# Kernel tuning notes

Measured on AMD Instinct MI355X. Metric: run time of the kernel, lower is better.

## Reference

```python
import jax, jax.numpy as jnp
import numpy as np

SEQ_LEN = 2048
DIM = 1024
HEADS = 16
DIM_HEAD = 64
INNER = HEADS * DIM_HEAD
BASE = 10000.0


def rope_tables(seq_len, head_dim):
    inv_freq = 1.0 / (BASE ** (jnp.arange(0, head_dim, 2, dtype=jnp.float32) / head_dim))
    t = jnp.arange(seq_len, dtype=jnp.float32)
    freqs = jnp.einsum('i,j->ij', t, inv_freq)          # [n, d/2]
    emb = jnp.concatenate([freqs, freqs], axis=-1)       # [n, d]
    return jnp.cos(emb), jnp.sin(emb)                    # each [n, d]


def rotate_half(x):
    d = x.shape[-1] // 2
    return jnp.concatenate([-x[..., d:], x[..., :d]], axis=-1)


def setup_inputs() -> dict:
    key = jax.random.key(0)
    ks = jax.random.split(key, 5)
    x = jax.random.normal(ks[0], (2, SEQ_LEN, DIM), dtype=jnp.float32)
    W_qkv = jax.random.normal(ks[1], (DIM, 3 * INNER), dtype=jnp.float32) * (DIM ** -0.5)
    W_out = jax.random.normal(ks[2], (INNER, DIM), dtype=jnp.float32) * (INNER ** -0.5)
    b_out = jnp.zeros((DIM,), dtype=jnp.float32)
    ln_g = jnp.ones((DIM,), dtype=jnp.float32)
    ln_b = jnp.zeros((DIM,), dtype=jnp.float32)
    return {"x": x, "W_qkv": W_qkv, "W_out": W_out, "b_out": b_out, "ln_g": ln_g, "ln_b": ln_b}


def reference(x, W_qkv, W_out, b_out, ln_g, ln_b):
    b, n, _ = x.shape
    # LayerNorm
    mu = jnp.mean(x, axis=-1, keepdims=True)
    var = jnp.mean(jnp.square(x - mu), axis=-1, keepdims=True)
    xn = (x - mu) * jax.lax.rsqrt(var + 1e-5) * ln_g + ln_b
    # QKV projection -> [b, h, n, d]
    qkv = xn @ W_qkv                                   # [b, n, 3*inner]
    q, k, v = jnp.split(qkv, 3, axis=-1)
    def to_heads(t):
        return t.reshape(b, n, HEADS, DIM_HEAD).transpose(0, 2, 1, 3)
    q, k, v = to_heads(q), to_heads(k), to_heads(v)
    # RoPE
    cos, sin = rope_tables(n, DIM_HEAD)                # [n, d]
    cos = cos[None, None]                              # [1,1,n,d]
    sin = sin[None, None]
    q = q * cos + rotate_half(q) * sin
    k = k * cos + rotate_half(k) * sin
    # Attention
    scale = DIM_HEAD ** -0.5
    dots = jnp.einsum('bhid,bhjd->bhij', q, k) * scale  # [b,h,n,n]
    causal = jnp.tril(jnp.ones((n, n), dtype=bool))
    dots = jnp.where(causal[None, None], dots, jnp.float32(-jnp.inf))
    attn = jax.nn.softmax(dots, axis=-1)
    out = jnp.einsum('bhij,bhjd->bhid', attn, v)       # [b,h,n,d]
    out = out.transpose(0, 2, 1, 3).reshape(b, n, INNER)
    return out @ W_out + b_out
```

## Files before the change

### kernel.cpp

```cpp
#include <hip/hip_runtime.h>
#include <hip/hip_bf16.h>

#define SEQ    2048
#define DMODEL 1024
#define HEADS  16
#define DHEAD  64
#define BATCH  2
#define TOK    (BATCH * SEQ)
#define NQKV   (3 * DMODEL)
#define QK_SCALE (0.125f * 1.4426950408889634f)

typedef __attribute__((ext_vector_type(8))) short bf16x8;
typedef __attribute__((ext_vector_type(4))) float f32x4;

__device__ __forceinline__ float bf2f(ushort u) {
  union { unsigned int i; float f; } v; v.i = ((unsigned int)u) << 16; return v.f;
}
__device__ __forceinline__ ushort f2bf(float f) {
  union { float f; unsigned int i; } v; v.f = f;
  unsigned int r = (v.i + 0x7fffu + ((v.i >> 16) & 1u)) >> 16;
  return (ushort)r;
}

__device__ __forceinline__ int swz(int row, int byteoff) {
  return row * 128 + (byteoff ^ ((row & 7) << 4));
}
__device__ __forceinline__ int kperm(int s) {
  return (s & 0x20) | ((s & 0x0C) << 1) | ((s & 0x10) >> 2) | (s & 3);
}

#define GLL16(g, l)                                                                     \
  __builtin_amdgcn_global_load_lds((const __attribute__((address_space(1))) void*)(g),  \
                                   (__attribute__((address_space(3))) void*)(l), 16, 0, 0)

__global__ __launch_bounds__(256) void ln_kernel(const float* __restrict__ x,
                                                 const float* __restrict__ g,
                                                 const float* __restrict__ b,
                                                 ushort* __restrict__ xn) {
  int t = blockIdx.x;
  int tid = threadIdx.x;
  const float* row = x + (size_t)t * DMODEL;
  float4 v = *(const float4*)(row + tid * 4);
  float s  = v.x + v.y + v.z + v.w;
  float s2 = v.x * v.x + v.y * v.y + v.z * v.z + v.w * v.w;
#pragma unroll
  for (int m = 32; m >= 1; m >>= 1) {
    s  += __shfl_down(s, m);
    s2 += __shfl_down(s2, m);
  }
  __shared__ float ws[4], ws2[4];
  if ((tid & 63) == 0) { ws[tid >> 6] = s; ws2[tid >> 6] = s2; }
  __syncthreads();
  s  = ws[0] + ws[1] + ws[2] + ws[3];
  s2 = ws2[0] + ws2[1] + ws2[2] + ws2[3];
  float mu  = s * (1.f / DMODEL);
  float var = s2 * (1.f / DMODEL) - mu * mu;
  float rs  = rsqrtf(var + 1e-5f);
  float4 gv = *(const float4*)(g + tid * 4);
  float4 bv = *(const float4*)(b + tid * 4);
  ushort4 o;
  o.x = f2bf((v.x - mu) * rs * gv.x + bv.x);
  o.y = f2bf((v.y - mu) * rs * gv.y + bv.y);
  o.z = f2bf((v.z - mu) * rs * gv.z + bv.z);
  o.w = f2bf((v.w - mu) * rs * gv.w + bv.w);
  *(ushort4*)(xn + (size_t)t * DMODEL + tid * 4) = o;
}

__global__ void transpose_f2b(const float* __restrict__ in, ushort* __restrict__ out,
                              int R, int C) {
  __shared__ float tile[32][33];
  int c0 = blockIdx.x * 32, r0 = blockIdx.y * 32;
  int x = threadIdx.x, y = threadIdx.y;
#pragma unroll
  for (int i = 0; i < 32; i += 8) tile[y + i][x] = in[(size_t)(r0 + y + i) * C + c0 + x];
  __syncthreads();
#pragma unroll
  for (int i = 0; i < 32; i += 8) out[(size_t)(c0 + y + i) * R + r0 + x] = f2bf(tile[x][y + i]);
}

__global__ void rope_tab_kernel(float* __restrict__ ct, float* __restrict__ st) {
  int n = blockIdx.x, d = threadIdx.x;
  float invf = expf(-logf(10000.f) * (float)(d & 31) * (1.f / 32.f));
  float a = (float)n * invf;
  ct[n * DHEAD + d] = cosf(a);
  st[n * DHEAD + d] = sinf(a);
}

template<int EPI>
__global__ __launch_bounds__(256) void gemm_bt(const ushort* __restrict__ A,
                                               const ushort* __restrict__ BT,
                                               float* __restrict__ Cf,
                                               const float* __restrict__ bias,
                                               ushort* __restrict__ qh,
                                               ushort* __restrict__ kh,
                                               ushort* __restrict__ vh,
                                               const float* __restrict__ ct,
                                               const float* __restrict__ st,
                                               int M, int N, int K) {
  __shared__ __align__(16) ushort As[128 * 64];
  __shared__ __align__(16) ushort Bs[128 * 64];
  int tid = threadIdx.x;
  int w = tid >> 6, lane = tid & 63;
  int lrow = lane & 15, g = lane >> 4;
  int gx = gridDim.x;
  int wg = blockIdx.x + gx * blockIdx.y;
  int nwg = gx * gridDim.y;
  int cpx = nwg >> 3;
  int swg = (wg & 7) * cpx + (wg >> 3);
  int m0 = (swg / gx) * 128, n0 = (swg % gx) * 128;
  int wr = (w >> 1) * 64, wc = (w & 1) * 64;
  int r8 = lane >> 3, s8 = lane & 7;
  int scol = (s8 ^ r8) * 8;
  f32x4 acc[4][4] = {};
  for (int k0 = 0; k0 < K; k0 += 64) {
    __syncthreads();
#pragma unroll
    for (int c = 0; c < 4; c++) {
      int row = w * 32 + c * 8;
      GLL16(A  + (size_t)(m0 + row + r8) * K + k0 + scol, As + row * 64);
      GLL16(BT + (size_t)(n0 + row + r8) * K + k0 + scol, Bs + row * 64);
    }
    __syncthreads();
#pragma unroll
    for (int ks = 0; ks < 2; ks++) {
      bf16x8 af[4], bf[4];
#pragma unroll
      for (int i = 0; i < 4; i++) {
        int ra = wr + i * 16 + lrow;
        af[i] = *(const bf16x8*)((const char*)As + swz(ra, g * 16 + ks * 64));
        int rb = wc + i * 16 + lrow;
        bf[i] = *(const bf16x8*)((const char*)Bs + swz(rb, g * 16 + ks * 64));
      }
      __builtin_amdgcn_s_setprio(1);
#pragma unroll
      for (int mf = 0; mf < 4; mf++)
#pragma unroll
        for (int nf = 0; nf < 4; nf++)
          acc[mf][nf] = __builtin_amdgcn_mfma_f32_16x16x32_bf16(af[mf], bf[nf], acc[mf][nf], 0, 0, 0);
      __builtin_amdgcn_s_setprio(0);
    }
  }
#pragma unroll
  for (int mf = 0; mf < 4; mf++)
#pragma unroll
    for (int nf = 0; nf < 4; nf++) {
      int col = n0 + wc + nf * 16 + lrow;
#pragma unroll
      for (int r = 0; r < 4; r++) {
        int rowi = m0 + wr + mf * 16 + g * 4 + r;
        float val = acc[mf][nf][r];
        if (EPI == 2) {
          Cf[(size_t)rowi * N + col] = val + bias[col];
        } else {
          int mat = col >> 10, c1 = col & 1023;
          int h = c1 >> 6, d = c1 & 63;
          int bb = rowi >> 11, n = rowi & (SEQ - 1);
          if (mat < 2) {
            float partner = acc[mf][nf ^ 2][r];
            float cs = ct[n * DHEAD + d], sn = st[n * DHEAD + d];
            float sgn = (d & 32) ? 1.f : -1.f;
            val = val * cs + sgn * partner * sn;
            if (mat == 0) val *= QK_SCALE;
          }
          ushort* dst = (mat == 0) ? qh : (mat == 1) ? kh : vh;
          dst[((size_t)(bb * HEADS + h) * SEQ + n) * DHEAD + d] = f2bf(val);
        }
      }
    }
}

__global__ __launch_bounds__(256) void attn_kernel(const ushort* __restrict__ q,
                                                   const ushort* __restrict__ k,
                                                   const ushort* __restrict__ v,
                                                   ushort* __restrict__ ao) {
  int wgid = blockIdx.x + gridDim.x * blockIdx.y;
  int j5 = wgid >> 3;
  int bh  = (wgid & 7) * 4 + (j5 >> 4);
  int pid = j5 & 15;
  int qlo = pid, qhi = (SEQ / 64 - 1) - pid;
  int tid = threadIdx.x, w = tid >> 6, lane = tid & 63;
  int lrow = lane & 15, g = lane >> 4;
  __shared__ __align__(16) ushort Ks[2][64 * 64];
  __shared__ __align__(16) ushort Vt[2][64 * 64];
  const ushort* qb = q + (size_t)bh * SEQ * DHEAD;
  const ushort* kb = k + (size_t)bh * SEQ * DHEAD;
  const ushort* vb = v + (size_t)bh * SEQ * DHEAD;
  const ushort* qph = qb + (size_t)(qhi * 64 + w * 16 + lrow) * DHEAD + g * 8;
  const ushort* qpl = qb + (size_t)(qlo * 64 + w * 16 + lrow) * DHEAD + g * 8;
  bf16x8 qh0 = *(const bf16x8*)(qph), qh1 = *(const bf16x8*)(qph + 32);
  bf16x8 ql0 = *(const bf16x8*)(qpl), ql1 = *(const bf16x8*)(qpl + 32);
  f32x4 aOh[4] = {}, aOl[4] = {};
  float l_hi = 0.f, l_lo = 0.f;

  int krow = tid >> 2, kco = (tid & 3) * 16;
  int pik = kperm(krow);
  int d0 = (tid & 31) * 2, kv8 = (tid >> 5) * 8;
  int4 ka0, ka1;
  unsigned int vd[8];

#define STAGE_ISSUE(j)                                                          \
  {                                                                             \
    const ushort* ks = kb + ((size_t)((j) * 64 + pik)) * DHEAD + kco;           \
    ka0 = *(const int4*)ks;                                                     \
    ka1 = *(const int4*)(ks + 8);                                               \
    const ushort* vs = vb + ((size_t)((j) * 64 + kv8)) * DHEAD + d0;            \
    _Pragma("unroll")                                                           \
    for (int jj = 0; jj < 8; jj++) vd[jj] = *(const unsigned int*)(vs + jj * DHEAD); \
  }

#define STAGE_WRITE(bsel)                                                       \
  {                                                                             \
    char* kd = (char*)Ks[bsel];                                                 \
    *(int4*)(kd + swz(krow, (tid & 3) * 32)) = ka0;                             \
    *(int4*)(kd + swz(krow, (tid & 3) * 32 + 16)) = ka1;                        \
    unsigned int lo[4], hi[4];                                                  \
    _Pragma("unroll")                                                           \
    for (int jj = 0; jj < 4; jj++) {                                            \
      lo[jj] = __builtin_amdgcn_perm(vd[2 * jj + 1], vd[2 * jj], 0x05040100u);  \
      hi[jj] = __builtin_amdgcn_perm(vd[2 * jj + 1], vd[2 * jj], 0x07060302u);  \
    }                                                                           \
    char* vdst = (char*)Vt[bsel];                                               \
    *(int4*)(vdst + swz(d0, kv8 * 2))     = *(int4*)lo;                         \
    *(int4*)(vdst + swz(d0 + 1, kv8 * 2)) = *(int4*)hi;                         \
  }

  STAGE_ISSUE(0);
  STAGE_WRITE(0);
  __syncthreads();
  int cur = 0;

  for (int jt = 0; jt <= qhi; jt++) {
    if (jt < qhi) STAGE_ISSUE(jt + 1);
    const char* kbuf = (const char*)Ks[cur];
    const char* vbuf = (const char*)Vt[cur];
    bf16x8 kf[8];
#pragma unroll
    for (int nf = 0; nf < 4; nf++) {
      kf[2 * nf]     = *(const bf16x8*)(kbuf + swz(nf * 16 + lrow, g * 16));
      kf[2 * nf + 1] = *(const bf16x8*)(kbuf + swz(nf * 16 + lrow, g * 16 + 64));
    }
    bf16x8 pah0, pah1, pal0, pal1;
    bool do_lo = (jt <= qlo);
    {
      f32x4 aS[4] = {};
      __builtin_amdgcn_s_setprio(1);
#pragma unroll
      for (int nf = 0; nf < 4; nf++) {
        aS[nf] = __builtin_amdgcn_mfma_f32_16x16x32_bf16(kf[2 * nf], qh0, aS[nf], 0, 0, 0);
        aS[nf] = __builtin_amdgcn_mfma_f32_16x16x32_bf16(kf[2 * nf + 1], qh1, aS[nf], 0, 0, 0);
      }
      __builtin_amdgcn_s_setprio(0);
      union { bf16x8 v; __hip_bfloat162 h[4]; } a0, a1;
      bool diag = (jt == qhi);
#pragma unroll
      for (int nf = 0; nf < 4; nf++) {
        float p[4];
#pragma unroll
        for (int r = 0; r < 4; r++) {
          int kvl = (nf >> 1) * 32 + g * 8 + (nf & 1) * 4 + r;
          p[r] = exp2f(aS[nf][r]);
          if (diag && kvl > w * 16 + lrow) p[r] = 0.f;
          l_hi += p[r];
        }
        __hip_bfloat162 plo = __float22bfloat162_rn({p[0], p[1]});
        __hip_bfloat162 phi = __float22bfloat162_rn({p[2], p[3]});
        if (nf < 2) { a0.h[(nf & 1) * 2] = plo; a0.h[(nf & 1) * 2 + 1] = phi; }
        else        { a1.h[(nf & 1) * 2] = plo; a1.h[(nf & 1) * 2 + 1] = phi; }
      }
      pah0 = a0.v; pah1 = a1.v;
    }
    if (do_lo) {
      f32x4 aS[4] = {};
      __builtin_amdgcn_s_setprio(1);
#pragma unroll
      for (int nf = 0; nf < 4; nf++) {
        aS[nf] = __builtin_amdgcn_mfma_f32_16x16x32_bf16(kf[2 * nf], ql0, aS[nf], 0, 0, 0);
        aS[nf] = __builtin_amdgcn_mfma_f32_16x16x32_bf16(kf[2 * nf + 1], ql1, aS[nf], 0, 0, 0);
      }
      __builtin_amdgcn_s_setprio(0);
      union { bf16x8 v; __hip_bfloat162 h[4]; } a0, a1;
      bool diag = (jt == qlo);
#pragma unroll
      for (int nf = 0; nf < 4; nf++) {
        float p[4];
#pragma unroll
        for (int r = 0; r < 4; r++) {
          int kvl = (nf >> 1) * 32 + g * 8 + (nf & 1) * 4 + r;
          p[r] = exp2f(aS[nf][r]);
          if (diag && kvl > w * 16 + lrow) p[r] = 0.f;
          l_lo += p[r];
        }
        __hip_bfloat162 plo = __float22bfloat162_rn({p[0], p[1]});
        __hip_bfloat162 phi = __float22bfloat162_rn({p[2], p[3]});
        if (nf < 2) { a0.h[(nf & 1) * 2] = plo; a0.h[(nf & 1) * 2 + 1] = phi; }
        else        { a1.h[(nf & 1) * 2] = plo; a1.h[(nf & 1) * 2 + 1] = phi; }
      }
      pal0 = a0.v; pal1 = a1.v;
    }
    bf16x8 vf[8];
#pragma unroll
    for (int nf = 0; nf < 4; nf++) {
      vf[2 * nf]     = *(const bf16x8*)(vbuf + swz(nf * 16 + lrow, g * 16));
      vf[2 * nf + 1] = *(const bf16x8*)(vbuf + swz(nf * 16 + lrow, g * 16 + 64));
    }
    __builtin_amdgcn_s_setprio(1);
#pragma unroll
    for (int nf = 0; nf < 4; nf++) {
      aOh[nf] = __builtin_amdgcn_mfma_f32_16x16x32_bf16(pah0, vf[2 * nf], aOh[nf], 0, 0, 0);
      aOh[nf] = __builtin_amdgcn_mfma_f32_16x16x32_bf16(pah1, vf[2 * nf + 1], aOh[nf], 0, 0, 0);
    }
    if (do_lo) {
#pragma unroll
      for (int nf = 0; nf < 4; nf++) {
        aOl[nf] = __builtin_amdgcn_mfma_f32_16x16x32_bf16(pal0, vf[2 * nf], aOl[nf], 0, 0, 0);
        aOl[nf] = __builtin_amdgcn_mfma_f32_16x16x32_bf16(pal1, vf[2 * nf + 1], aOl[nf], 0, 0, 0);
      }
    }
    __builtin_amdgcn_s_setprio(0);
    if (jt < qhi) STAGE_WRITE(cur ^ 1);
    __syncthreads();
    cur ^= 1;
  }

  l_hi += __shfl_xor(l_hi, 16); l_hi += __shfl_xor(l_hi, 32);
  l_lo += __shfl_xor(l_lo, 16); l_lo += __shfl_xor(l_lo, 32);
  int b = bh >> 4, h = bh & 15;
#pragma unroll
  for (int r = 0; r < 4; r++) {
    float ih = 1.f / __shfl(l_hi, g * 4 + r);
    float il = 1.f / __shfl(l_lo, g * 4 + r);
#pragma unroll
    for (int nf = 0; nf < 4; nf++) {
      int col = h * DHEAD + nf * 16 + lrow;
      int th = b * SEQ + qhi * 64 + w * 16 + g * 4 + r;
      int tl = b * SEQ + qlo * 64 + w * 16 + g * 4 + r;
      ao[(size_t)th * DMODEL + col] = f2bf(aOh[nf][r] * ih);
      ao[(size_t)tl * DMODEL + col] = f2bf(aOl[nf][r] * il);
    }
  }
#undef STAGE_ISSUE
#undef STAGE_WRITE
}

extern "C" void kernel_launch(void* const* d_in, const int* in_sizes, int n_in,
                              void* d_out, int out_size, void* d_ws, size_t ws_size,
                              hipStream_t stream) {
  const float* x    = (const float*)d_in[0];
  const float* Wqkv = (const float*)d_in[1];
  const float* Wout = (const float*)d_in[2];
  const float* bout = (const float*)d_in[3];
  const float* lng  = (const float*)d_in[4];
  const float* lnb  = (const float*)d_in[5];
  float* out = (float*)d_out;

  ushort* xn    = (ushort*)d_ws;
  ushort* WqkvT = xn + (size_t)TOK * DMODEL;
  ushort* WoutT = WqkvT + (size_t)NQKV * DMODEL;
  ushort* qh    = WoutT + (size_t)DMODEL * DMODEL;
  ushort* kh    = qh + (size_t)BATCH * HEADS * SEQ * DHEAD;
  ushort* vh    = kh + (size_t)BATCH * HEADS * SEQ * DHEAD;
  float*  ct    = (float*)(vh + (size_t)BATCH * HEADS * SEQ * DHEAD);
  float*  st    = ct + SEQ * DHEAD;
  ushort* ao    = xn;

  hipLaunchKernelGGL(ln_kernel, dim3(TOK), dim3(256), 0, stream, x, lng, lnb, xn);
  hipLaunchKernelGGL(transpose_f2b, dim3(NQKV / 32, DMODEL / 32), dim3(32, 8), 0, stream,
                     Wqkv, WqkvT, DMODEL, NQKV);
  hipLaunchKernelGGL(transpose_f2b, dim3(DMODEL / 32, DMODEL / 32), dim3(32, 8), 0, stream,
                     Wout, WoutT, DMODEL, DMODEL);
  hipLaunchKernelGGL(rope_tab_kernel, dim3(SEQ), dim3(DHEAD), 0, stream, ct, st);
  hipLaunchKernelGGL(gemm_bt<1>, dim3(NQKV / 128, TOK / 128), dim3(256), 0, stream,
                     xn, WqkvT, (float*)nullptr, (const float*)nullptr,
                     qh, kh, vh, ct, st, TOK, NQKV, DMODEL);
  hipLaunchKernelGGL(attn_kernel, dim3(16, BATCH * HEADS), dim3(256), 0, stream,
                     qh, kh, vh, ao);
  hipLaunchKernelGGL(gemm_bt<2>, dim3(DMODEL / 128, TOK / 128), dim3(256), 0, stream,
                     ao, WoutT, out, bout,
                     (ushort*)nullptr, (ushort*)nullptr, (ushort*)nullptr,
                     (const float*)nullptr, (const float*)nullptr, TOK, DMODEL, DMODEL);
}
```

Before: 146.9 us.

## Halve GEMM K-tile to 32 and drop workgroup swizzle

Shrinks the GEMM K-step from 64 to 32, which halves the LDS tiles and changes the global-to-LDS load pattern and the XOR swizzle to a 32-wide row layout. It also removes the grouped workgroup remapping that was meant to improve L2 locality, and uses a plain blockIdx mapping instead. The smaller LDS footprint may allow more resident blocks. In exchange it doubles the number of barrier pairs per K, gives each barrier less MFMA work to overlap, and may lose the cache reuse the remapping provided.

```diff
diff --git a/kernel.cpp b/kernel.cpp
--- a/kernel.cpp
+++ b/kernel.cpp
@@ -97,48 +97,40 @@
                                                const float* __restrict__ ct,
                                                const float* __restrict__ st,
                                                int M, int N, int K) {
-  __shared__ __align__(16) ushort As[128 * 64];
-  __shared__ __align__(16) ushort Bs[128 * 64];
+  __shared__ __align__(16) ushort As[128 * 32];
+  __shared__ __align__(16) ushort Bs[128 * 32];
   int tid = threadIdx.x;
   int w = tid >> 6, lane = tid & 63;
   int lrow = lane & 15, g = lane >> 4;
-  int gx = gridDim.x;
-  int wg = blockIdx.x + gx * blockIdx.y;
-  int nwg = gx * gridDim.y;
-  int cpx = nwg >> 3;
-  int swg = (wg & 7) * cpx + (wg >> 3);
-  int m0 = (swg / gx) * 128, n0 = (swg % gx) * 128;
+  int m0 = blockIdx.y * 128, n0 = blockIdx.x * 128;
   int wr = (w >> 1) * 64, wc = (w & 1) * 64;
-  int r8 = lane >> 3, s8 = lane & 7;
-  int scol = (s8 ^ r8) * 8;
+  int grow = lane >> 2;
+  int gcol = ((lane & 3) ^ ((grow >> 1) & 3)) * 8;
+  ushort* ldsA0 = As + w * 512;
+  ushort* ldsA1 = As + 2048 + w * 512;
+  ushort* ldsB0 = Bs + w * 512;
+  ushort* ldsB1 = Bs + 2048 + w * 512;
+  int fcol = (g ^ ((lrow >> 1) & 3)) * 8;
   f32x4 acc[4][4] = {};
-  for (int k0 = 0; k0 < K; k0 += 64) {
+  for (int k0 = 0; k0 < K; k0 += 32) {
     __syncthreads();
-#pragma unroll
-    for (int c = 0; c < 4; c++) {
-      int row = w * 32 + c * 8;
-      GLL16(A  + (size_t)(m0 + row + r8) * K + k0 + scol, As + row * 64);
-      GLL16(BT + (size_t)(n0 + row + r8) * K + k0 + scol, Bs + row * 64);
-    }
+    GLL16(A  + (size_t)(m0 + w * 16 + grow) * K + k0 + gcol, ldsA0);
+    GLL16(A  + (size_t)(m0 + 64 + w * 16 + grow) * K + k0 + gcol, ldsA1);
+    GLL16(BT + (size_t)(n0 + w * 16 + grow) * K + k0 + gcol, ldsB0);
+    GLL16(BT + (size_t)(n0 + 64 + w * 16 + grow) * K + k0 + gcol, ldsB1);
     __syncthreads();
-#pragma unroll
-    for (int ks = 0; ks < 2; ks++) {
-      bf16x8 af[4], bf[4];
-#pragma unroll
-      for (int i = 0; i < 4; i++) {
-        int ra = wr + i * 16 + lrow;
-        af[i] = *(const bf16x8*)((const char*)As + swz(ra, g * 16 + ks * 64));
-        int rb = wc + i * 16 + lrow;
-        bf[i] = *(const bf16x8*)((const char*)Bs + swz(rb, g * 16 + ks * 64));
-      }
-      __builtin_amdgcn_s_setprio(1);
-#pragma unroll
-      for (int mf = 0; mf < 4; mf++)
-#pragma unroll
-        for (int nf = 0; nf < 4; nf++)
-          acc[mf][nf] = __builtin_amdgcn_mfma_f32_16x16x32_bf16(af[mf], bf[nf], acc[mf][nf], 0, 0, 0);
-      __builtin_amdgcn_s_setprio(0);
-    }
+    bf16x8 af[4], bfr[4];
+#pragma unroll
+    for (int i = 0; i < 4; i++) af[i]  = *(const bf16x8*)(As + (wr + i * 16 + lrow) * 32 + fcol);
+#pragma unroll
+    for (int i = 0; i < 4; i++) bfr[i] = *(const bf16x8*)(Bs + (wc + i * 16 + lrow) * 32 + fcol);
+    __builtin_amdgcn_s_setprio(1);
+#pragma unroll
+    for (int mf = 0; mf < 4; mf++)
+#pragma unroll
+      for (int nf = 0; nf < 4; nf++)
+        acc[mf][nf] = __builtin_amdgcn_mfma_f32_16x16x32_bf16(af[mf], bfr[nf], acc[mf][nf], 0, 0, 0);
+    __builtin_amdgcn_s_setprio(0);
   }
 #pragma unroll
   for (int mf = 0; mf < 4; mf++)
```

Result: faster. 135.3 us (-7.9%).
